# Optimization experiments

Hardware: AMD Instinct MI355X
Metric: run time of the kernel (lower is better)

Reference implementation:

```python
import jax, jax.numpy as jnp
import numpy as np

SIREN_OMEGA_0 = 30.0
EPS = 1e-4


def setup_inputs() -> dict:
    key = jax.random.key(0)
    ks = jax.random.split(key, 10)
    B, N, M, IN, OUT = 2, 16384, 1024, 256, 256
    x = jax.random.normal(ks[0], (B, N, IN), dtype=jnp.float32)
    query_coords = jax.random.normal(ks[1], (B, N, 3), dtype=jnp.float32)
    atomic_coords = jax.random.normal(ks[2], (B, M, 3), dtype=jnp.float32)
    # SIREN init (not is_first): bound = sqrt(6/in)/omega_0
    bound = (6.0 / IN) ** 0.5 / SIREN_OMEGA_0
    W = jax.random.uniform(ks[3], (OUT, IN), jnp.float32, -bound, bound)
    b = jax.random.uniform(ks[4], (OUT,), jnp.float32, -bound, bound)
    # freq_net: Linear(3,16) -> Softplus -> Linear(16,1), default torch init
    b1l = 1.0 / np.sqrt(3.0)
    fw1 = jax.random.uniform(ks[5], (16, 3), jnp.float32, -b1l, b1l)
    fb1 = jax.random.uniform(ks[6], (16,), jnp.float32, -b1l, b1l)
    b2l = 1.0 / np.sqrt(16.0)
    fw2 = jax.random.uniform(ks[7], (1, 16), jnp.float32, -b2l, b2l)
    fb2 = jax.random.uniform(ks[8], (1,), jnp.float32, -b2l, b2l)
    return {"x": x, "query_coords": query_coords, "atomic_coords": atomic_coords,
            "W": W, "b": b, "fw1": fw1, "fb1": fb1, "fw2": fw2, "fb2": fb2}


def reference(x, query_coords, atomic_coords, W, b, fw1, fb1, fw2, fb2):
    omega_base = SIREN_OMEGA_0
    # pre_activation = x @ W^T + b : [B, N, OUT]
    pre = jnp.einsum('bni,oi->bno', x, W) + b
    # freq_net(query_coords): Linear -> softplus -> Linear, clamp [0,5], nan->0
    h = jax.nn.softplus(jnp.einsum('bnd,hd->bnh', query_coords, fw1) + fb1)
    local_scale = jnp.einsum('bnh,oh->bno', h, fw2) + fb2  # [B, N, 1]
    local_scale = jnp.nan_to_num(jnp.clip(local_scale, 0.0, 5.0), nan=0.0)
    # pairwise distance [B, N, M] via broadcasted diff, then min over atoms
    diff = query_coords[:, :, None, :] - atomic_coords[:, None, :, :]  # [B,N,M,3]
    dist = jnp.sqrt(jnp.maximum(jnp.sum(diff * diff, axis=-1), EPS))
    min_dist = jnp.min(dist, axis=-1, keepdims=True)  # [B, N, 1]
    omega = omega_base * (1.0 + local_scale * jnp.exp(-min_dist))
    return jnp.sin(omega * pre)
```

## Files before the change

kernel.cpp:

```cpp
#include <hip/hip_runtime.h>
#include <hip/hip_bf16.h>

#define NPTS    32768
#define K_DIM   256
#define O_DIM   256
#define M_ATOMS 1024

typedef __attribute__((ext_vector_type(8))) short short8;
typedef __attribute__((ext_vector_type(4))) float f32x4;

__device__ __forceinline__ unsigned short bf16_rn(float f) {
  unsigned u = __float_as_uint(f);
  unsigned r = u + 0x7FFFu + ((u >> 16) & 1u);
  return (unsigned short)(r >> 16);
}

__device__ __forceinline__ void cvt8(const f32x4 f0, const f32x4 f1,
                                     short8* h, short8* l) {
#pragma unroll
  for (int j = 0; j < 4; ++j) {
    unsigned short h0 = bf16_rn(f0[j]);
    (*h)[j] = (short)h0;
    (*l)[j] = (short)bf16_rn(f0[j] - __uint_as_float((unsigned)h0 << 16));
    unsigned short h1 = bf16_rn(f1[j]);
    (*h)[j + 4] = (short)h1;
    (*l)[j + 4] = (short)bf16_rn(f1[j] - __uint_as_float((unsigned)h1 << 16));
  }
}

__device__ __forceinline__ void async16(void* l, const void* g) {
  __builtin_amdgcn_global_load_lds(
      (const __attribute__((address_space(1))) void*)g,
      (__attribute__((address_space(3))) void*)l, 16, 0, 0);
}

__global__ __launch_bounds__(256) void wprep_kernel(const float* __restrict__ W,
                                                    unsigned short* __restrict__ whF,
                                                    unsigned short* __restrict__ wlF) {
  int t = blockIdx.x * 256 + threadIdx.x;
  int lane = t & 63;
  int ct = (t >> 6) & 15;
  int kc = t >> 10;
  int col = ct * 16 + (lane & 15);
  int k0 = kc * 32 + (lane >> 4) * 8;
  const float* src = W + (size_t)col * K_DIM + k0;
  f32x4 f0 = *(const f32x4*)(src);
  f32x4 f1 = *(const f32x4*)(src + 4);
  short8 h, l;
  cvt8(f0, f1, &h, &l);
  *(short8*)(whF + (size_t)t * 8) = h;
  *(short8*)(wlF + (size_t)t * 8) = l;
}

__global__ __launch_bounds__(256, 2) void fused_kernel(
    const float* __restrict__ x, const float* __restrict__ qc,
    const float* __restrict__ atoms,
    const unsigned short* __restrict__ whF, const unsigned short* __restrict__ wlF,
    const float* __restrict__ bias,
    const float* __restrict__ fw1, const float* __restrict__ fb1,
    const float* __restrict__ fw2, const float* __restrict__ fb2,
    float* __restrict__ out) {
  __shared__ f32x4 bsh[2][2048];
  char* ldsC = (char*)&bsh[0][0];
  const int lane = threadIdx.x & 63;
  const int wave = threadIdx.x >> 6;
  const int ptile = wave >> 1;
  const int ch = wave & 1;
  const int lrow = lane & 15;
  const int lk = lane >> 4;
  const int pbase = blockIdx.x * 64 + ptile * 32;

  float bias_r[8];
#pragma unroll
  for (int ct = 0; ct < 8; ++ct) bias_r[ct] = bias[(ch * 8 + ct) * 16 + lrow];

  const char* whB = (const char*)whF;
  const char* wlB = (const char*)wlF;
  const int toff = wave * 1024 + lane * 16;

  {
    char* db = ldsC;
    const char* gh = whB + toff;
    const char* gl = wlB + toff;
#pragma unroll
    for (int j = 0; j < 4; ++j) {
      async16(db + j * 4096 + wave * 1024, gh + j * 4096);
      async16(db + 16384 + j * 4096 + wave * 1024, gl + j * 4096);
    }
  }

  const float* xr0 = x + (size_t)(pbase + lrow) * K_DIM + lk * 8;
  const float* xr1 = x + (size_t)(pbase + 16 + lrow) * K_DIM + lk * 8;
  f32x4 a00 = *(const f32x4*)(xr0), a01 = *(const f32x4*)(xr0 + 4);
  f32x4 a10 = *(const f32x4*)(xr1), a11 = *(const f32x4*)(xr1 + 4);
  short8 ahi0, alo0, ahi1, alo1;
  cvt8(a00, a01, &ahi0, &alo0);
  cvt8(a10, a11, &ahi1, &alo1);

  f32x4 acc[16];
#pragma unroll
  for (int i = 0; i < 16; ++i) acc[i] = (f32x4){0.f, 0.f, 0.f, 0.f};

  __syncthreads();

  int cur = 0;
  f32x4 n00, n01, n10, n11;
#pragma unroll 1
  for (int it = 0; it < 8; ++it) {
    if (it < 7) {
      char* db = ldsC + (cur ^ 1) * 32768;
      const char* gh = whB + (it + 1) * 16384 + toff;
      const char* gl = wlB + (it + 1) * 16384 + toff;
#pragma unroll
      for (int j = 0; j < 4; ++j) {
        async16(db + j * 4096 + wave * 1024, gh + j * 4096);
        async16(db + 16384 + j * 4096 + wave * 1024, gl + j * 4096);
      }
      const float* p0 = xr0 + (it + 1) * 32;
      const float* p1 = xr1 + (it + 1) * 32;
      n00 = *(const f32x4*)(p0); n01 = *(const f32x4*)(p0 + 4);
      n10 = *(const f32x4*)(p1); n11 = *(const f32x4*)(p1 + 4);
    }
    const char* bp = ldsC + cur * 32768 + ch * 8192;
#pragma unroll
    for (int ct = 0; ct < 8; ++ct) {
      short8 bh = *(const short8*)(bp + ct * 1024 + lane * 16);
      short8 bl = *(const short8*)(bp + 16384 + ct * 1024 + lane * 16);
      acc[ct]     = __builtin_amdgcn_mfma_f32_16x16x32_bf16(ahi0, bh, acc[ct],     0, 0, 0);
      acc[8 + ct] = __builtin_amdgcn_mfma_f32_16x16x32_bf16(ahi1, bh, acc[8 + ct], 0, 0, 0);
      acc[ct]     = __builtin_amdgcn_mfma_f32_16x16x32_bf16(alo0, bh, acc[ct],     0, 0, 0);
      acc[8 + ct] = __builtin_amdgcn_mfma_f32_16x16x32_bf16(alo1, bh, acc[8 + ct], 0, 0, 0);
      acc[ct]     = __builtin_amdgcn_mfma_f32_16x16x32_bf16(ahi0, bl, acc[ct],     0, 0, 0);
      acc[8 + ct] = __builtin_amdgcn_mfma_f32_16x16x32_bf16(ahi1, bl, acc[8 + ct], 0, 0, 0);
    }
    __syncthreads();
    if (it < 7) {
      cvt8(n00, n01, &ahi0, &alo0);
      cvt8(n10, n11, &ahi1, &alo1);
      cur ^= 1;
    }
  }

  const int batch = pbase >> 14;
  const float* A = atoms + (size_t)batch * M_ATOMS * 3;
  f32x4* at4 = (f32x4*)ldsC;
  float* red = (float*)(ldsC + 16384);
  for (int i = threadIdx.x; i < M_ATOMS; i += 256) {
    const float* ap = A + i * 3;
    float ax = ap[0], ay = ap[1], az = ap[2];
    f32x4 v = {ax, ay, az, ax * ax + ay * ay + az * az};
    at4[i] = v;
  }
  __syncthreads();

  const int p = lane & 31;
  const int pt = pbase + p;
  const float qx = qc[(size_t)pt * 3 + 0];
  const float qy = qc[(size_t)pt * 3 + 1];
  const float qz = qc[(size_t)pt * 3 + 2];
  float m0 = 3.0e38f, m1 = 3.0e38f, m2 = 3.0e38f, m3 = 3.0e38f;
  const int i0 = (ch * 2 + (lane >> 5)) * 256;
  for (int i = i0; i < i0 + 256; i += 4) {
    f32x4 v0 = at4[i + 0], v1 = at4[i + 1], v2 = at4[i + 2], v3 = at4[i + 3];
    float d;
    d = v0[0] * qx; d = __fmaf_rn(v0[1], qy, d); d = __fmaf_rn(v0[2], qz, d);
    m0 = fminf(m0, __fmaf_rn(d, -2.0f, v0[3]));
    d = v1[0] * qx; d = __fmaf_rn(v1[1], qy, d); d = __fmaf_rn(v1[2], qz, d);
    m1 = fminf(m1, __fmaf_rn(d, -2.0f, v1[3]));
    d = v2[0] * qx; d = __fmaf_rn(v2[1], qy, d); d = __fmaf_rn(v2[2], qz, d);
    m2 = fminf(m2, __fmaf_rn(d, -2.0f, v2[3]));
    d = v3[0] * qx; d = __fmaf_rn(v3[1], qy, d); d = __fmaf_rn(v3[2], qz, d);
    m3 = fminf(m3, __fmaf_rn(d, -2.0f, v3[3]));
  }
  float md = fminf(fminf(m0, m1), fminf(m2, m3));
  red[wave * 64 + lane] = md;
  __syncthreads();
  {
    const int rb = ptile * 128;
    md = fminf(fminf(red[rb + p], red[rb + 32 + p]),
               fminf(red[rb + 64 + p], red[rb + 96 + p]));
  }
  md += qx * qx + qy * qy + qz * qz;
  float mind = sqrtf(fmaxf(md, 1.0e-4f));

  float facc = fb2[0];
#pragma unroll
  for (int j = 0; j < 16; ++j) {
    float z = fw1[j * 3 + 0] * qx + fw1[j * 3 + 1] * qy + fw1[j * 3 + 2] * qz + fb1[j];
    facc += fw2[j] * log1pf(__expf(z));
  }
  float ls = fminf(fmaxf(facc, 0.0f), 5.0f);
  float omega_l = 30.0f * (1.0f + ls * __expf(-mind));

  float om[2][4];
#pragma unroll
  for (int t = 0; t < 2; ++t)
#pragma unroll
    for (int j = 0; j < 4; ++j)
      om[t][j] = __shfl(omega_l, t * 16 + lk * 4 + j);

#pragma unroll
  for (int ct = 0; ct < 8; ++ct) {
#pragma unroll
    for (int t = 0; t < 2; ++t) {
#pragma unroll
      for (int j = 0; j < 4; ++j) {
        float pre = acc[t * 8 + ct][j] + bias_r[ct];
        out[(size_t)(pbase + t * 16 + lk * 4 + j) * O_DIM + (ch * 8 + ct) * 16 + lrow] =
            __sinf(om[t][j] * pre);
      }
    }
  }
}

extern "C" void kernel_launch(void* const* d_in, const int* in_sizes, int n_in,
                              void* d_out, int out_size, void* d_ws, size_t ws_size,
                              hipStream_t stream) {
  (void)in_sizes; (void)n_in; (void)out_size; (void)ws_size;
  const float* x     = (const float*)d_in[0];
  const float* qc    = (const float*)d_in[1];
  const float* atoms = (const float*)d_in[2];
  const float* W     = (const float*)d_in[3];
  const float* b     = (const float*)d_in[4];
  const float* fw1   = (const float*)d_in[5];
  const float* fb1   = (const float*)d_in[6];
  const float* fw2   = (const float*)d_in[7];
  const float* fb2   = (const float*)d_in[8];
  float* out = (float*)d_out;

  unsigned short* whF = (unsigned short*)d_ws;
  unsigned short* wlF = whF + 65536;

  wprep_kernel<<<32, 256, 0, stream>>>(W, whF, wlF);
  fused_kernel<<<512, 256, 0, stream>>>(x, qc, atoms, whF, wlF, b,
                                        fw1, fb1, fw2, fb2, out);
}
```

Baseline: 120.7 us.

## Split output columns across blocks and stage each block's W slice fully in LDS

Each block now handles 256 points and a 64-column quarter of the output using 512 threads. The block's entire hi/lo bf16 W slice is loaded into LDS once, which removes the per-iteration double-buffer syncs. Each wave computes 32 points by 64 columns, and the atom min-distance reduction becomes a single cross-lane shuffle instead of an LDS reduction. The catch is that x rows, the min-distance search and the freq-net work are now recomputed by four blocks per point group, and the larger LDS footprint may limit occupancy.

```diff
diff --git a/kernel.cpp b/kernel.cpp
--- a/kernel.cpp
+++ b/kernel.cpp
@@ -9,22 +9,22 @@
 typedef __attribute__((ext_vector_type(8))) short short8;
 typedef __attribute__((ext_vector_type(4))) float f32x4;
 
-__device__ __forceinline__ unsigned short bf16_rn(float f) {
-  unsigned u = __float_as_uint(f);
-  unsigned r = u + 0x7FFFu + ((u >> 16) & 1u);
-  return (unsigned short)(r >> 16);
+__device__ __forceinline__ void split1(float v, short* h, short* l) {
+  unsigned short hu = __bfloat16_as_ushort(__float2bfloat16(v));
+  *h = (short)hu;
+  float r = v - __uint_as_float((unsigned)hu << 16);
+  *l = (short)__bfloat16_as_ushort(__float2bfloat16(r));
 }
 
 __device__ __forceinline__ void cvt8(const f32x4 f0, const f32x4 f1,
                                      short8* h, short8* l) {
 #pragma unroll
   for (int j = 0; j < 4; ++j) {
-    unsigned short h0 = bf16_rn(f0[j]);
-    (*h)[j] = (short)h0;
-    (*l)[j] = (short)bf16_rn(f0[j] - __uint_as_float((unsigned)h0 << 16));
-    unsigned short h1 = bf16_rn(f1[j]);
-    (*h)[j + 4] = (short)h1;
-    (*l)[j + 4] = (short)bf16_rn(f1[j] - __uint_as_float((unsigned)h1 << 16));
+    short hh, ll;
+    split1(f0[j], &hh, &ll);
+    (*h)[j] = hh; (*l)[j] = ll;
+    split1(f1[j], &hh, &ll);
+    (*h)[j + 4] = hh; (*l)[j + 4] = ll;
   }
 }
 
@@ -52,7 +52,7 @@
   *(short8*)(wlF + (size_t)t * 8) = l;
 }
 
-__global__ __launch_bounds__(256, 2) void fused_kernel(
+__global__ __launch_bounds__(512, 4) void fused_kernel(
     const float* __restrict__ x, const float* __restrict__ qc,
     const float* __restrict__ atoms,
     const unsigned short* __restrict__ whF, const unsigned short* __restrict__ wlF,
@@ -60,107 +60,99 @@
     const float* __restrict__ fw1, const float* __restrict__ fb1,
     const float* __restrict__ fw2, const float* __restrict__ fb2,
     float* __restrict__ out) {
-  __shared__ f32x4 bsh[2][2048];
-  char* ldsC = (char*)&bsh[0][0];
+  __shared__ char lds[65536];
   const int lane = threadIdx.x & 63;
-  const int wave = threadIdx.x >> 6;
-  const int ptile = wave >> 1;
-  const int ch = wave & 1;
+  const int w = threadIdx.x >> 6;
   const int lrow = lane & 15;
   const int lk = lane >> 4;
-  const int pbase = blockIdx.x * 64 + ptile * 32;
-
-  float bias_r[8];
-#pragma unroll
-  for (int ct = 0; ct < 8; ++ct) bias_r[ct] = bias[(ch * 8 + ct) * 16 + lrow];
-
-  const char* whB = (const char*)whF;
-  const char* wlB = (const char*)wlF;
-  const int toff = wave * 1024 + lane * 16;
+  const int pb = (int)(blockIdx.x >> 2) * 256;
+  const int cq = blockIdx.x & 3;
+  const int pbase = pb + w * 32;
 
   {
-    char* db = ldsC;
-    const char* gh = whB + toff;
-    const char* gl = wlB + toff;
-#pragma unroll
-    for (int j = 0; j < 4; ++j) {
-      async16(db + j * 4096 + wave * 1024, gh + j * 4096);
-      async16(db + 16384 + j * 4096 + wave * 1024, gl + j * 4096);
-    }
-  }
+    const char* whB = (const char*)whF;
+    const char* wlB = (const char*)wlF;
+    const int t = threadIdx.x;
+    const int inner = (t & 255) * 16;
+    const int kco = t >> 8;
+#pragma unroll
+    for (int p = 0; p < 4; ++p) {
+      const int kc = p * 2 + kco;
+      async16(lds + kc * 4096 + inner,
+              whB + kc * 16384 + cq * 4096 + inner);
+      async16(lds + 32768 + kc * 4096 + inner,
+              wlB + kc * 16384 + cq * 4096 + inner);
+    }
+  }
+
+  float bias_r[4];
+#pragma unroll
+  for (int ct = 0; ct < 4; ++ct) bias_r[ct] = bias[cq * 64 + ct * 16 + lrow];
 
   const float* xr0 = x + (size_t)(pbase + lrow) * K_DIM + lk * 8;
-  const float* xr1 = x + (size_t)(pbase + 16 + lrow) * K_DIM + lk * 8;
-  f32x4 a00 = *(const f32x4*)(xr0), a01 = *(const f32x4*)(xr0 + 4);
-  f32x4 a10 = *(const f32x4*)(xr1), a11 = *(const f32x4*)(xr1 + 4);
-  short8 ahi0, alo0, ahi1, alo1;
-  cvt8(a00, a01, &ahi0, &alo0);
-  cvt8(a10, a11, &ahi1, &alo1);
-
-  f32x4 acc[16];
-#pragma unroll
-  for (int i = 0; i < 16; ++i) acc[i] = (f32x4){0.f, 0.f, 0.f, 0.f};
+  const float* xr1 = xr0 + 16 * K_DIM;
+
+  f32x4 c00 = *(const f32x4*)(xr0);
+  f32x4 c01 = *(const f32x4*)(xr0 + 4);
+  f32x4 c10 = *(const f32x4*)(xr1);
+  f32x4 c11 = *(const f32x4*)(xr1 + 4);
+
+  f32x4 acc[2][4];
+#pragma unroll
+  for (int t = 0; t < 2; ++t)
+#pragma unroll
+    for (int ct = 0; ct < 4; ++ct) acc[t][ct] = (f32x4){0.f, 0.f, 0.f, 0.f};
 
   __syncthreads();
 
-  int cur = 0;
-  f32x4 n00, n01, n10, n11;
 #pragma unroll 1
-  for (int it = 0; it < 8; ++it) {
-    if (it < 7) {
-      char* db = ldsC + (cur ^ 1) * 32768;
-      const char* gh = whB + (it + 1) * 16384 + toff;
-      const char* gl = wlB + (it + 1) * 16384 + toff;
-#pragma unroll
-      for (int j = 0; j < 4; ++j) {
-        async16(db + j * 4096 + wave * 1024, gh + j * 4096);
-        async16(db + 16384 + j * 4096 + wave * 1024, gl + j * 4096);
-      }
-      const float* p0 = xr0 + (it + 1) * 32;
-      const float* p1 = xr1 + (it + 1) * 32;
+  for (int kc = 0; kc < 8; ++kc) {
+    f32x4 n00, n01, n10, n11;
+    if (kc < 7) {
+      const float* p0 = xr0 + (kc + 1) * 32;
+      const float* p1 = xr1 + (kc + 1) * 32;
       n00 = *(const f32x4*)(p0); n01 = *(const f32x4*)(p0 + 4);
       n10 = *(const f32x4*)(p1); n11 = *(const f32x4*)(p1 + 4);
     }
-    const char* bp = ldsC + cur * 32768 + ch * 8192;
-#pragma unroll
-    for (int ct = 0; ct < 8; ++ct) {
+    short8 ahi0, alo0, ahi1, alo1;
+    cvt8(c00, c01, &ahi0, &alo0);
+    cvt8(c10, c11, &ahi1, &alo1);
+    const char* bp = lds + kc * 4096;
+#pragma unroll
+    for (int ct = 0; ct < 4; ++ct) {
       short8 bh = *(const short8*)(bp + ct * 1024 + lane * 16);
-      short8 bl = *(const short8*)(bp + 16384 + ct * 1024 + lane * 16);
-      acc[ct]     = __builtin_amdgcn_mfma_f32_16x16x32_bf16(ahi0, bh, acc[ct],     0, 0, 0);
-      acc[8 + ct] = __builtin_amdgcn_mfma_f32_16x16x32_bf16(ahi1, bh, acc[8 + ct], 0, 0, 0);
-      acc[ct]     = __builtin_amdgcn_mfma_f32_16x16x32_bf16(alo0, bh, acc[ct],     0, 0, 0);
-      acc[8 + ct] = __builtin_amdgcn_mfma_f32_16x16x32_bf16(alo1, bh, acc[8 + ct], 0, 0, 0);
-      acc[ct]     = __builtin_amdgcn_mfma_f32_16x16x32_bf16(ahi0, bl, acc[ct],     0, 0, 0);
-      acc[8 + ct] = __builtin_amdgcn_mfma_f32_16x16x32_bf16(ahi1, bl, acc[8 + ct], 0, 0, 0);
-    }
-    __syncthreads();
-    if (it < 7) {
-      cvt8(n00, n01, &ahi0, &alo0);
-      cvt8(n10, n11, &ahi1, &alo1);
-      cur ^= 1;
-    }
-  }
-
-  const int batch = pbase >> 14;
+      short8 bl = *(const short8*)(bp + 32768 + ct * 1024 + lane * 16);
+      acc[0][ct] = __builtin_amdgcn_mfma_f32_16x16x32_bf16(ahi0, bh, acc[0][ct], 0, 0, 0);
+      acc[1][ct] = __builtin_amdgcn_mfma_f32_16x16x32_bf16(ahi1, bh, acc[1][ct], 0, 0, 0);
+      acc[0][ct] = __builtin_amdgcn_mfma_f32_16x16x32_bf16(alo0, bh, acc[0][ct], 0, 0, 0);
+      acc[1][ct] = __builtin_amdgcn_mfma_f32_16x16x32_bf16(alo1, bh, acc[1][ct], 0, 0, 0);
+      acc[0][ct] = __builtin_amdgcn_mfma_f32_16x16x32_bf16(ahi0, bl, acc[0][ct], 0, 0, 0);
+      acc[1][ct] = __builtin_amdgcn_mfma_f32_16x16x32_bf16(ahi1, bl, acc[1][ct], 0, 0, 0);
+    }
+    c00 = n00; c01 = n01; c10 = n10; c11 = n11;
+  }
+
+  __syncthreads();
+  const int batch = pb >> 14;
   const float* A = atoms + (size_t)batch * M_ATOMS * 3;
-  f32x4* at4 = (f32x4*)ldsC;
-  float* red = (float*)(ldsC + 16384);
-  for (int i = threadIdx.x; i < M_ATOMS; i += 256) {
+  f32x4* at4 = (f32x4*)lds;
+  {
+    int i = threadIdx.x * 2;
     const float* ap = A + i * 3;
     float ax = ap[0], ay = ap[1], az = ap[2];
-    f32x4 v = {ax, ay, az, ax * ax + ay * ay + az * az};
-    at4[i] = v;
+    at4[i] = (f32x4){ax, ay, az, ax * ax + ay * ay + az * az};
+    ax = ap[3]; ay = ap[4]; az = ap[5];
+    at4[i + 1] = (f32x4){ax, ay, az, ax * ax + ay * ay + az * az};
   }
   __syncthreads();
 
-  const int p = lane & 31;
-  const int pt = pbase + p;
+  const int pt = pbase + (lane & 31);
   const float qx = qc[(size_t)pt * 3 + 0];
   const float qy = qc[(size_t)pt * 3 + 1];
   const float qz = qc[(size_t)pt * 3 + 2];
   float m0 = 3.0e38f, m1 = 3.0e38f, m2 = 3.0e38f, m3 = 3.0e38f;
-  const int i0 = (ch * 2 + (lane >> 5)) * 256;
-  for (int i = i0; i < i0 + 256; i += 4) {
+  const int i0 = (lane >> 5) * 512;
+  for (int i = i0; i < i0 + 512; i += 4) {
     f32x4 v0 = at4[i + 0], v1 = at4[i + 1], v2 = at4[i + 2], v3 = at4[i + 3];
     float d;
     d = v0[0] * qx; d = __fmaf_rn(v0[1], qy, d); d = __fmaf_rn(v0[2], qz, d);
@@ -173,13 +165,7 @@
     m3 = fminf(m3, __fmaf_rn(d, -2.0f, v3[3]));
   }
   float md = fminf(fminf(m0, m1), fminf(m2, m3));
-  red[wave * 64 + lane] = md;
-  __syncthreads();
-  {
-    const int rb = ptile * 128;
-    md = fminf(fminf(red[rb + p], red[rb + 32 + p]),
-               fminf(red[rb + 64 + p], red[rb + 96 + p]));
-  }
+  md = fminf(md, __shfl_xor(md, 32));
   md += qx * qx + qy * qy + qz * qz;
   float mind = sqrtf(fmaxf(md, 1.0e-4f));
 
@@ -200,13 +186,13 @@
       om[t][j] = __shfl(omega_l, t * 16 + lk * 4 + j);
 
 #pragma unroll
-  for (int ct = 0; ct < 8; ++ct) {
-#pragma unroll
-    for (int t = 0; t < 2; ++t) {
+  for (int t = 0; t < 2; ++t) {
+#pragma unroll
+    for (int ct = 0; ct < 4; ++ct) {
 #pragma unroll
       for (int j = 0; j < 4; ++j) {
-        float pre = acc[t * 8 + ct][j] + bias_r[ct];
-        out[(size_t)(pbase + t * 16 + lk * 4 + j) * O_DIM + (ch * 8 + ct) * 16 + lrow] =
+        float pre = acc[t][ct][j] + bias_r[ct];
+        out[(size_t)(pbase + t * 16 + lk * 4 + j) * O_DIM + cq * 64 + ct * 16 + lrow] =
             __sinf(om[t][j] * pre);
       }
     }
@@ -232,6 +218,6 @@
   unsigned short* wlF = whF + 65536;
 
   wprep_kernel<<<32, 256, 0, stream>>>(W, whF, wlF);
-  fused_kernel<<<512, 256, 0, stream>>>(x, qc, atoms, whF, wlF, b,
+  fused_kernel<<<512, 512, 0, stream>>>(x, qc, atoms, whF, wlF, b,
                                         fw1, fb1, fw2, fb2, out);
 }
```

After: 136.1 us. 1.13x slower.
